# Kernel optimization log

Hardware: AMD Instinct MI355X
Metric: run time of the kernel (lower is better)

Reference implementation:

```python
import jax, jax.numpy as jnp
import numpy as np
import math

N_SSM = 64
DIRECTIONS = 4

def setup_inputs() -> dict:
    key = jax.random.key(0)
    ks = jax.random.split(key, 10)
    S, B, E = 1024, 16, 1024
    H, N = DIRECTIONS * N_SSM, 2  # kernel_dim, ndim
    d = {}
    d['x'] = jax.random.normal(ks[0], (S, B, E), jnp.float32)
    for i, name in enumerate(['A_1', 'A_2', 'A_3', 'A_4']):
        d[name] = 0.2 * jax.random.normal(ks[1 + i], (H, N), jnp.float32)
    d['B_1'] = 0.2 * jax.random.normal(ks[5], (H, N), jnp.float32)
    d['B_2'] = 0.2 * jax.random.normal(ks[6], (H, N), jnp.float32)
    d['C_1'] = jax.random.normal(ks[7], (H, N), jnp.float32)
    d['C_2'] = jax.random.normal(ks[8], (H, N), jnp.float32)
    d['omega'] = jax.random.normal(ks[9], (E,), jnp.float32)
    return d


def _compute_kernel(A_1, A_2, A_3, A_4, B_1, B_2, C_1, C_2, Ls):
    # 2D SSM impulse response on an Ls x Ls grid (real, diagonal state dim N).
    # Recurrence (input = delta at (0,0)):
    #   x_h[i,j] = A1*x_h[i,j-1] + A2*x_v[i,j-1] + B1*u[i,j]
    #   x_v[i,j] = A3*x_h[i-1,j] + A4*x_v[i-1,j] + B2*u[i,j]
    #   k[i,j]   = scale*(C1.x_h[i,j] + C2.x_v[i,j])
    H, N = A_1.shape
    scale = math.sqrt(1.0 / N)
    A1, A2 = jax.nn.sigmoid(A_1), jax.nn.sigmoid(A_2)
    A3, A4 = jax.nn.sigmoid(A_3), jax.nn.sigmoid(A_4)
    B1, B2 = jax.nn.sigmoid(B_1), jax.nn.sigmoid(B_2)
    zeros_row = jnp.zeros((Ls, H, N), A1.dtype)

    def row_step(carry, i):
        xh_prev, xv_prev = carry  # [Ls, H, N] from row i-1
        first = (i == 0).astype(A1.dtype)
        xv_row = A3 * xh_prev + A4 * xv_prev
        xv_row = xv_row.at[0].add(first * B2)
        xv_shift = jnp.concatenate([jnp.zeros((1, H, N), A1.dtype), xv_row[:-1]], axis=0)
        c = A2 * xv_shift
        c = c.at[0].add(first * B1)

        def col_step(xh_left, cj):
            xh = A1 * xh_left + cj
            return xh, xh

        _, xh_row = jax.lax.scan(col_step, jnp.zeros((H, N), A1.dtype), c)
        y_row = scale * (jnp.einsum('lhn,hn->lh', xh_row, C_1)
                         + jnp.einsum('lhn,hn->lh', xv_row, C_2))
        return (xh_row, xv_row), y_row

    _, K = jax.lax.scan(row_step, (zeros_row, zeros_row), jnp.arange(Ls))  # [Ls, Ls, H]
    # boundary corrections from the original code
    K = K.at[0, :, :].multiply(2.0)
    K = K.at[:, 0, :].multiply(2.0)
    K = K.at[0, 0].divide(4.0)
    return K  # [Ls, Ls, H]


def _fft_conv2d(xd, kd, Ls):
    # xd: [B, E, Ls, Ls], kd: [E, Ls, Ls] -> linear 2D conv via zero-padded FFT
    s = (2 * Ls, 2 * Ls)
    kf = jnp.fft.rfft2(kd, s=s)          # [E, 2Ls, Ls+1]
    xf = jnp.fft.rfft2(xd, s=s)          # [B, E, 2Ls, Ls+1]
    y = jnp.fft.irfft2(xf * kf, s=s)
    return y[..., :Ls, :Ls]


def reference(x, A_1, A_2, A_3, A_4, B_1, B_2, C_1, C_2, omega):
    S, B, E = x.shape
    Ls = int(math.isqrt(S))
    H = C_1.shape[0]                      # kernel_dim = directions * n_ssm
    n_ssm = H // DIRECTIONS
    rep = E // n_ssm

    residual = x * omega                  # [S, B, E]
    x4 = x.transpose(1, 2, 0).reshape(B, E, Ls, Ls)

    K = _compute_kernel(A_1, A_2, A_3, A_4, B_1, B_2, C_1, C_2, Ls)  # [Ls, Ls, H]
    K = K.transpose(2, 0, 1)              # [H, Ls, Ls]

    flip_dims = [(), (-2,), (-1,), (-2, -1)]
    out = jnp.zeros_like(x4)
    for d, flips in enumerate(flip_dims):
        kd = jnp.tile(K[d * n_ssm:(d + 1) * n_ssm], (rep, 1, 1))  # [E, Ls, Ls]
        xd = jnp.flip(x4, axis=flips) if flips else x4
        y = _fft_conv2d(xd, kd, Ls)
        out = out + (jnp.flip(y, axis=flips) if flips else y)

    out = out.reshape(B, E, S).transpose(2, 0, 1)  # [S, B, E]
    return jax.nn.silu(out + residual)
```

## Files before the change

### kernel.cpp

```cpp
#include <hip/hip_runtime.h>
#include <hip/hip_fp16.h>


#define NPB 8
#define THREADS 256
#define M_TOT 16384
#define SCALE 0.70710678118654752f

typedef __attribute__((ext_vector_type(2))) _Float16 v2h;

__device__ __forceinline__ unsigned h2u(v2h v) { return __builtin_bit_cast(unsigned, v); }
__device__ __forceinline__ v2h u2h(unsigned v) { return __builtin_bit_cast(v2h, v); }
__device__ __forceinline__ v2h hfma2v(v2h a, v2h b, v2h c) {
    return __builtin_elementwise_fma(a, b, c);
}
__device__ __forceinline__ v2h cvt2(float x, float y) {
    return (v2h){(_Float16)x, (_Float16)y};
}

template<int CTRL>
__device__ __forceinline__ v2h dpph(v2h v) {
    return u2h((unsigned)__builtin_amdgcn_update_dpp(
        0, (int)h2u(v), CTRL, 0xF, 0xF, true));
}
__device__ __forceinline__ float swzrev(float v) {
    return __int_as_float(__builtin_amdgcn_ds_swizzle(__float_as_int(v), 0x7C1F));
}
__device__ __forceinline__ float sigm(float v) { return 1.0f / (1.0f + __expf(-v)); }

struct DirPH {
    v2h a1, p2, p4, p8, w;
    v2h a2z, ab, a3, a4, b1, b2, a3b1, c1, c2;
    float k00;
};

__device__ __forceinline__ void dir_init_h(DirPH& P, int h, int j,
    const float* __restrict__ A1p, const float* __restrict__ A2p,
    const float* __restrict__ A3p, const float* __restrict__ A4p,
    const float* __restrict__ B1p, const float* __restrict__ B2p,
    const float* __restrict__ C1p, const float* __restrict__ C2p)
{
    float2 a1r = *(const float2*)(A1p + 2 * h);
    float2 a2r = *(const float2*)(A2p + 2 * h);
    float2 a3r = *(const float2*)(A3p + 2 * h);
    float2 a4r = *(const float2*)(A4p + 2 * h);
    float2 b1r = *(const float2*)(B1p + 2 * h);
    float2 b2r = *(const float2*)(B2p + 2 * h);
    float2 c1r = *(const float2*)(C1p + 2 * h);
    float2 c2r = *(const float2*)(C2p + 2 * h);
    float a1v0 = sigm(a1r.x), a1v1 = sigm(a1r.y);
    float p2v0 = a1v0 * a1v0, p2v1 = a1v1 * a1v1;
    float p4v0 = p2v0 * p2v0, p4v1 = p2v1 * p2v1;
    float p8v0 = p4v0 * p4v0, p8v1 = p4v1 * p4v1;
    float a3v0 = sigm(a3r.x), a3v1 = sigm(a3r.y);
    float a4v0 = sigm(a4r.x), a4v1 = sigm(a4r.y);
    float b1v0 = sigm(b1r.x), b1v1 = sigm(b1r.y);
    float b2v0 = sigm(b2r.x), b2v1 = sigm(b2r.y);
    float c1v0 = SCALE * c1r.x, c1v1 = SCALE * c1r.y;
    float c2v0 = SCALE * c2r.x, c2v1 = SCALE * c2r.y;
    P.a1 = cvt2(a1v0, a1v1); P.p2 = cvt2(p2v0, p2v1);
    P.p4 = cvt2(p4v0, p4v1); P.p8 = cvt2(p8v0, p8v1);
    P.a3 = cvt2(a3v0, a3v1); P.a4 = cvt2(a4v0, a4v1);
    P.b1 = cvt2(b1v0, b1v1); P.b2 = cvt2(b2v0, b2v1);
    P.a3b1 = cvt2(a3v0 * b1v0, a3v1 * b1v1);
    P.c1 = cvt2(c1v0, c1v1); P.c2 = cvt2(c2v0, c2v1);
    P.k00 = c1v0 * b1v0 + c1v1 * b1v1 + c2v0 * b2v0 + c2v1 * b2v1;
    const bool edge = (j == 0);
    float z0 = edge ? 0.f : sigm(a2r.x);
    float z1 = edge ? 0.f : sigm(a2r.y);
    P.a2z = cvt2(z0, z1);
    P.ab  = cvt2(z0 * b2v0, z1 * b2v1);
    float e = (float)((j & 15) + 1);
    P.w = cvt2(__powf(a1v0, e), __powf(a1v1, e));
}

__device__ __forceinline__ void dir_pre_h(const DirPH& P, v2h u2, v2h up2,
    v2h xh, v2h xv, v2h cx, v2h& nxv, v2h& ncx, v2h& d, v2h& e)
{
    v2h b2u = P.b2 * u2;
    nxv = hfma2v(P.a3, xh, hfma2v(P.a4, xv, b2u));
    ncx = hfma2v(P.a3b1, up2, hfma2v(P.a4, cx, b2u));
    v2h xl = dpph<0x138>(nxv);
    v2h ul = dpph<0x138>(u2);
    v2h b1u = P.b1 * u2;
    d = hfma2v(P.a2z, xl, b1u);
    e = hfma2v(P.ab, ul, b1u);
}

__device__ __forceinline__ float dir_post_h(const DirPH& P, v2h nh, v2h rh,
    v2h nxv, v2h ncx, v2h& xh, v2h& xv, v2h& cx, float base)
{
    v2h s1 = nh + rh;
    v2h s2 = nxv + ncx;
    float y = __builtin_amdgcn_fdot2(P.c1, s1,
              __builtin_amdgcn_fdot2(P.c2, s2, base, false), false);
    xh = nh; xv = nxv; cx = ncx;
    return y;
}

__device__ __forceinline__ void scan4h(
    unsigned& f0, unsigned& f1, unsigned& r0, unsigned& r1,
    const DirPH& PF, const DirPH& PR)
{
    asm("s_nop 1\n\t"
        "v_pk_fmac_f16_dpp %0, %0, %4  row_shr:1 row_mask:0xf bank_mask:0xf bound_ctrl:0\n\t"
        "v_pk_fmac_f16_dpp %1, %1, %4  row_shr:1 row_mask:0xf bank_mask:0xf bound_ctrl:0\n\t"
        "v_pk_fmac_f16_dpp %2, %2, %9  row_shr:1 row_mask:0xf bank_mask:0xf bound_ctrl:0\n\t"
        "v_pk_fmac_f16_dpp %3, %3, %9  row_shr:1 row_mask:0xf bank_mask:0xf bound_ctrl:0\n\t"
        "v_pk_fmac_f16_dpp %0, %0, %5  row_shr:2 row_mask:0xf bank_mask:0xf bound_ctrl:0\n\t"
        "v_pk_fmac_f16_dpp %1, %1, %5  row_shr:2 row_mask:0xf bank_mask:0xf bound_ctrl:0\n\t"
        "v_pk_fmac_f16_dpp %2, %2, %10 row_shr:2 row_mask:0xf bank_mask:0xf bound_ctrl:0\n\t"
        "v_pk_fmac_f16_dpp %3, %3, %10 row_shr:2 row_mask:0xf bank_mask:0xf bound_ctrl:0\n\t"
        "v_pk_fmac_f16_dpp %0, %0, %6  row_shr:4 row_mask:0xf bank_mask:0xf bound_ctrl:0\n\t"
        "v_pk_fmac_f16_dpp %1, %1, %6  row_shr:4 row_mask:0xf bank_mask:0xf bound_ctrl:0\n\t"
        "v_pk_fmac_f16_dpp %2, %2, %11 row_shr:4 row_mask:0xf bank_mask:0xf bound_ctrl:0\n\t"
        "v_pk_fmac_f16_dpp %3, %3, %11 row_shr:4 row_mask:0xf bank_mask:0xf bound_ctrl:0\n\t"
        "v_pk_fmac_f16_dpp %0, %0, %7  row_shr:8 row_mask:0xf bank_mask:0xf bound_ctrl:0\n\t"
        "v_pk_fmac_f16_dpp %1, %1, %7  row_shr:8 row_mask:0xf bank_mask:0xf bound_ctrl:0\n\t"
        "v_pk_fmac_f16_dpp %2, %2, %12 row_shr:8 row_mask:0xf bank_mask:0xf bound_ctrl:0\n\t"
        "v_pk_fmac_f16_dpp %3, %3, %12 row_shr:8 row_mask:0xf bank_mask:0xf bound_ctrl:0\n\t"
        "v_pk_fmac_f16_dpp %0, %0, %8  row_bcast:15 row_mask:0xa bank_mask:0xf bound_ctrl:0\n\t"
        "v_pk_fmac_f16_dpp %1, %1, %8  row_bcast:15 row_mask:0xa bank_mask:0xf bound_ctrl:0\n\t"
        "v_pk_fmac_f16_dpp %2, %2, %13 row_bcast:15 row_mask:0xa bank_mask:0xf bound_ctrl:0\n\t"
        "v_pk_fmac_f16_dpp %3, %3, %13 row_bcast:15 row_mask:0xa bank_mask:0xf bound_ctrl:0"
        : "+v"(f0), "+v"(f1), "+v"(r0), "+v"(r1)
        : "v"(h2u(PF.a1)), "v"(h2u(PF.p2)), "v"(h2u(PF.p4)),
          "v"(h2u(PF.p8)), "v"(h2u(PF.w)),
          "v"(h2u(PR.a1)), "v"(h2u(PR.p2)), "v"(h2u(PR.p4)),
          "v"(h2u(PR.p8)), "v"(h2u(PR.w)));
}

__global__ __launch_bounds__(THREADS) void ssm2d_kernel(
    const float* __restrict__ x,
    const float* __restrict__ A1p, const float* __restrict__ A2p,
    const float* __restrict__ A3p, const float* __restrict__ A4p,
    const float* __restrict__ B1p, const float* __restrict__ B2p,
    const float* __restrict__ C1p, const float* __restrict__ C2p,
    const float* __restrict__ omega,
    float* __restrict__ out)
{
    __shared__ _Float16 u_lds[NPB * 1024];
    __shared__ _Float16 a_lds[NPB * 1024];
    const int t = threadIdx.x;
    const int bid = blockIdx.x;
    const int m0  = ((bid & 7) * 256 + (bid >> 3)) * NPB;

    const int simg = t & 7;
    #pragma unroll 4
    for (int it = 0; it < 32; ++it) {
        int pix = it * 32 + (t >> 3);
        u_lds[simg * 1024 + (pix ^ (simg << 2))] =
            (_Float16)x[(size_t)pix * M_TOT + (m0 + simg)];
    }
    __syncthreads();

    const int j    = t & 31;
    const int img  = t >> 5;
    const int m    = m0 + img;
    const int hb   = m & 63;
    const int colx = j ^ (img << 2);
    const int colr = 31 ^ colx;
    const _Float16* uim = u_lds + img * 1024;
    _Float16*       aim = a_lds + img * 1024;
    const float om = omega[m & 1023];

    {
        DirPH P0, P2;
        dir_init_h(P0, hb,       j, A1p, A2p, A3p, A4p, B1p, B2p, C1p, C2p);
        dir_init_h(P2, 128 + hb, j, A1p, A2p, A3p, A4p, B1p, B2p, C1p, C2p);
        const float omA = om - P0.k00;
        v2h xhF = {0,0}, xvF = {0,0}, cxF = {0,0};
        v2h xhR = {0,0}, xvR = {0,0}, cxR = {0,0};
        v2h up2 = {0,0}, upr2 = {0,0};
        #pragma unroll 4
        for (int s = 0; s < 32; ++s) {
            _Float16 uh  = uim[s * 32 + colx];
            _Float16 urh = uim[s * 32 + colr];
            float uf = (float)uh, urf = (float)urh;
            v2h u2  = (v2h){uh, uh};
            v2h ur2 = (v2h){urh, urh};
            v2h nxvF, ncxF, dF, eF, nxvR, ncxR, dR, eR;
            dir_pre_h(P0, u2,  up2,  xhF, xvF, cxF, nxvF, ncxF, dF, eF);
            dir_pre_h(P2, ur2, upr2, xhR, xvR, cxR, nxvR, ncxR, dR, eR);
            unsigned f0 = h2u(dF), f1 = h2u(eF), r0 = h2u(dR), r1 = h2u(eR);
            scan4h(f0, f1, r0, r1, P0, P2);
            float y0 = dir_post_h(P0, u2h(f0), u2h(f1), nxvF, ncxF,
                                  xhF, xvF, cxF, 0.f);
            float y2 = dir_post_h(P2, u2h(r0), u2h(r1), nxvR, ncxR,
                                  xhR, xvR, cxR, -P2.k00 * urf);
            float y2f = swzrev(y2);
            aim[s * 32 + colx] = (_Float16)fmaf(uf, omA, y0 + y2f);
            up2 = u2; upr2 = ur2;
        }
    }
    {
        DirPH P1, P3;
        dir_init_h(P1, 64 + hb,  j, A1p, A2p, A3p, A4p, B1p, B2p, C1p, C2p);
        dir_init_h(P3, 192 + hb, j, A1p, A2p, A3p, A4p, B1p, B2p, C1p, C2p);
        v2h xhF = {0,0}, xvF = {0,0}, cxF = {0,0};
        v2h xhR = {0,0}, xvR = {0,0}, cxR = {0,0};
        v2h up2 = {0,0}, upr2 = {0,0};
        #pragma unroll 4
        for (int s = 0; s < 32; ++s) {
            int   r   = 31 - s;
            _Float16 uh  = uim[r * 32 + colx];
            _Float16 urh = uim[r * 32 + colr];
            float uf = (float)uh, urf = (float)urh;
            v2h u2  = (v2h){uh, uh};
            v2h ur2 = (v2h){urh, urh};
            v2h nxvF, ncxF, dF, eF, nxvR, ncxR, dR, eR;
            dir_pre_h(P1, u2,  up2,  xhF, xvF, cxF, nxvF, ncxF, dF, eF);
            dir_pre_h(P3, ur2, upr2, xhR, xvR, cxR, nxvR, ncxR, dR, eR);
            unsigned f0 = h2u(dF), f1 = h2u(eF), r0 = h2u(dR), r1 = h2u(eR);
            scan4h(f0, f1, r0, r1, P1, P3);
            float y1 = dir_post_h(P1, u2h(f0), u2h(f1), nxvF, ncxF,
                                  xhF, xvF, cxF, 0.f);
            float y3 = dir_post_h(P3, u2h(r0), u2h(r1), nxvR, ncxR,
                                  xhR, xvR, cxR, -P3.k00 * urf);
            float y3f = swzrev(y3);
            float z  = (float)aim[r * 32 + colx] + y1 + y3f;
            z = fmaf(uf, -P1.k00, z);
            float sg = 1.0f / (1.0f + __expf(-z));
            aim[r * 32 + colx] = (_Float16)(z * sg);
            up2 = u2; upr2 = ur2;
        }
    }
    __syncthreads();

    #pragma unroll 4
    for (int it = 0; it < 32; ++it) {
        int pix = it * 32 + (t >> 3);
        out[(size_t)pix * M_TOT + (m0 + simg)] =
            (float)a_lds[simg * 1024 + (pix ^ (simg << 2))];
    }
}

extern "C" void kernel_launch(void* const* d_in, const int* in_sizes, int n_in,
                              void* d_out, int out_size, void* d_ws, size_t ws_size,
                              hipStream_t stream) {
    const float* x  = (const float*)d_in[0];
    const float* A1 = (const float*)d_in[1];
    const float* A2 = (const float*)d_in[2];
    const float* A3 = (const float*)d_in[3];
    const float* A4 = (const float*)d_in[4];
    const float* B1 = (const float*)d_in[5];
    const float* B2 = (const float*)d_in[6];
    const float* C1 = (const float*)d_in[7];
    const float* C2 = (const float*)d_in[8];
    const float* om = (const float*)d_in[9];
    float* out = (float*)d_out;
    hipLaunchKernelGGL(ssm2d_kernel, dim3(M_TOT / NPB), dim3(THREADS), 0, stream,
                       x, A1, A2, A3, A4, B1, B2, C1, C2, om, out);
}
```

Measured before the change: 210.7 us.

## Run forward and flipped direction pairs in separate warps, combine in LDS

Doubles the block to 512 threads so each image gets two warps: one runs the forward/reverse pair (directions 0,2) and the other the row-flipped pair (1,3) concurrently instead of sequentially. Each writes partial sums to its own fp16 LDS buffer, and the final store loop adds the two partials and applies SiLU. This halves the per-warp serial scan length and raises parallelism, at the cost of double LDS for partials, an extra fp16 rounding of the second partial, and potentially lower occupancy.

```diff
diff --git a/kernel.cpp b/kernel.cpp
--- a/kernel.cpp
+++ b/kernel.cpp
@@ -3,7 +3,7 @@
 
 
 #define NPB 8
-#define THREADS 256
+#define THREADS 512
 #define M_TOT 16384
 #define SCALE 0.70710678118654752f
 
@@ -140,98 +140,71 @@
     float* __restrict__ out)
 {
     __shared__ _Float16 u_lds[NPB * 1024];
-    __shared__ _Float16 a_lds[NPB * 1024];
+    __shared__ _Float16 p_lds[2 * NPB * 1024];
     const int t = threadIdx.x;
     const int bid = blockIdx.x;
     const int m0  = ((bid & 7) * 256 + (bid >> 3)) * NPB;
 
     const int simg = t & 7;
     #pragma unroll 4
-    for (int it = 0; it < 32; ++it) {
-        int pix = it * 32 + (t >> 3);
+    for (int it = 0; it < 16; ++it) {
+        int pix = it * 64 + (t >> 3);
         u_lds[simg * 1024 + (pix ^ (simg << 2))] =
             (_Float16)x[(size_t)pix * M_TOT + (m0 + simg)];
     }
     __syncthreads();
 
     const int j    = t & 31;
-    const int img  = t >> 5;
+    const int slot = t >> 5;
+    const int img  = slot >> 1;
+    const int flip = slot & 1;
     const int m    = m0 + img;
     const int hb   = m & 63;
     const int colx = j ^ (img << 2);
     const int colr = 31 ^ colx;
+    const int fmask = flip ? 31 : 0;
     const _Float16* uim = u_lds + img * 1024;
-    _Float16*       aim = a_lds + img * 1024;
+    _Float16*       pim = p_lds + flip * (NPB * 1024) + img * 1024;
     const float om = omega[m & 1023];
 
-    {
-        DirPH P0, P2;
-        dir_init_h(P0, hb,       j, A1p, A2p, A3p, A4p, B1p, B2p, C1p, C2p);
-        dir_init_h(P2, 128 + hb, j, A1p, A2p, A3p, A4p, B1p, B2p, C1p, C2p);
-        const float omA = om - P0.k00;
-        v2h xhF = {0,0}, xvF = {0,0}, cxF = {0,0};
-        v2h xhR = {0,0}, xvR = {0,0}, cxR = {0,0};
-        v2h up2 = {0,0}, upr2 = {0,0};
-        #pragma unroll 4
-        for (int s = 0; s < 32; ++s) {
-            _Float16 uh  = uim[s * 32 + colx];
-            _Float16 urh = uim[s * 32 + colr];
-            float uf = (float)uh, urf = (float)urh;
-            v2h u2  = (v2h){uh, uh};
-            v2h ur2 = (v2h){urh, urh};
-            v2h nxvF, ncxF, dF, eF, nxvR, ncxR, dR, eR;
-            dir_pre_h(P0, u2,  up2,  xhF, xvF, cxF, nxvF, ncxF, dF, eF);
-            dir_pre_h(P2, ur2, upr2, xhR, xvR, cxR, nxvR, ncxR, dR, eR);
-            unsigned f0 = h2u(dF), f1 = h2u(eF), r0 = h2u(dR), r1 = h2u(eR);
-            scan4h(f0, f1, r0, r1, P0, P2);
-            float y0 = dir_post_h(P0, u2h(f0), u2h(f1), nxvF, ncxF,
-                                  xhF, xvF, cxF, 0.f);
-            float y2 = dir_post_h(P2, u2h(r0), u2h(r1), nxvR, ncxR,
-                                  xhR, xvR, cxR, -P2.k00 * urf);
-            float y2f = swzrev(y2);
-            aim[s * 32 + colx] = (_Float16)fmaf(uf, omA, y0 + y2f);
-            up2 = u2; upr2 = ur2;
-        }
-    }
-    {
-        DirPH P1, P3;
-        dir_init_h(P1, 64 + hb,  j, A1p, A2p, A3p, A4p, B1p, B2p, C1p, C2p);
-        dir_init_h(P3, 192 + hb, j, A1p, A2p, A3p, A4p, B1p, B2p, C1p, C2p);
-        v2h xhF = {0,0}, xvF = {0,0}, cxF = {0,0};
-        v2h xhR = {0,0}, xvR = {0,0}, cxR = {0,0};
-        v2h up2 = {0,0}, upr2 = {0,0};
-        #pragma unroll 4
-        for (int s = 0; s < 32; ++s) {
-            int   r   = 31 - s;
-            _Float16 uh  = uim[r * 32 + colx];
-            _Float16 urh = uim[r * 32 + colr];
-            float uf = (float)uh, urf = (float)urh;
-            v2h u2  = (v2h){uh, uh};
-            v2h ur2 = (v2h){urh, urh};
-            v2h nxvF, ncxF, dF, eF, nxvR, ncxR, dR, eR;
-            dir_pre_h(P1, u2,  up2,  xhF, xvF, cxF, nxvF, ncxF, dF, eF);
-            dir_pre_h(P3, ur2, upr2, xhR, xvR, cxR, nxvR, ncxR, dR, eR);
-            unsigned f0 = h2u(dF), f1 = h2u(eF), r0 = h2u(dR), r1 = h2u(eR);
-            scan4h(f0, f1, r0, r1, P1, P3);
-            float y1 = dir_post_h(P1, u2h(f0), u2h(f1), nxvF, ncxF,
-                                  xhF, xvF, cxF, 0.f);
-            float y3 = dir_post_h(P3, u2h(r0), u2h(r1), nxvR, ncxR,
-                                  xhR, xvR, cxR, -P3.k00 * urf);
-            float y3f = swzrev(y3);
-            float z  = (float)aim[r * 32 + colx] + y1 + y3f;
-            z = fmaf(uf, -P1.k00, z);
-            float sg = 1.0f / (1.0f + __expf(-z));
-            aim[r * 32 + colx] = (_Float16)(z * sg);
-            up2 = u2; upr2 = ur2;
-        }
+    DirPH PF, PR;
+    dir_init_h(PF, hb + (flip << 6),       j, A1p, A2p, A3p, A4p, B1p, B2p, C1p, C2p);
+    dir_init_h(PR, 128 + hb + (flip << 6), j, A1p, A2p, A3p, A4p, B1p, B2p, C1p, C2p);
+    const float cF = (flip ? 0.f : om) - PF.k00;
+
+    v2h xhF = {0,0}, xvF = {0,0}, cxF = {0,0};
+    v2h xhR = {0,0}, xvR = {0,0}, cxR = {0,0};
+    v2h up2 = {0,0}, upr2 = {0,0};
+    #pragma unroll 4
+    for (int s = 0; s < 32; ++s) {
+        const int rr = s ^ fmask;
+        _Float16 uh  = uim[rr * 32 + colx];
+        _Float16 urh = uim[rr * 32 + colr];
+        float uf = (float)uh, urf = (float)urh;
+        v2h u2  = (v2h){uh, uh};
+        v2h ur2 = (v2h){urh, urh};
+        v2h nxvF, ncxF, dF, eF, nxvR, ncxR, dR, eR;
+        dir_pre_h(PF, u2,  up2,  xhF, xvF, cxF, nxvF, ncxF, dF, eF);
+        dir_pre_h(PR, ur2, upr2, xhR, xvR, cxR, nxvR, ncxR, dR, eR);
+        unsigned f0 = h2u(dF), f1 = h2u(eF), r0 = h2u(dR), r1 = h2u(eR);
+        scan4h(f0, f1, r0, r1, PF, PR);
+        float yF = dir_post_h(PF, u2h(f0), u2h(f1), nxvF, ncxF,
+                              xhF, xvF, cxF, 0.f);
+        float yR = dir_post_h(PR, u2h(r0), u2h(r1), nxvR, ncxR,
+                              xhR, xvR, cxR, -PR.k00 * urf);
+        float yRf = swzrev(yR);
+        pim[rr * 32 + colx] = (_Float16)fmaf(uf, cF, yF + yRf);
+        up2 = u2; upr2 = ur2;
     }
     __syncthreads();
 
     #pragma unroll 4
-    for (int it = 0; it < 32; ++it) {
-        int pix = it * 32 + (t >> 3);
-        out[(size_t)pix * M_TOT + (m0 + simg)] =
-            (float)a_lds[simg * 1024 + (pix ^ (simg << 2))];
+    for (int it = 0; it < 16; ++it) {
+        int pix = it * 64 + (t >> 3);
+        int idx = simg * 1024 + (pix ^ (simg << 2));
+        float z  = (float)p_lds[idx] + (float)p_lds[NPB * 1024 + idx];
+        float sg = 1.0f / (1.0f + __expf(-z));
+        out[(size_t)pix * M_TOT + (m0 + simg)] = z * sg;
     }
 }
 
```

Result: faster. 204.9 us (-2.8%).
